# Optimization experiments

Measured on AMD Instinct MI355X. Metric: run time of the kernel, lower is better.

The kernel has to match this reference:

```python
import jax, jax.numpy as jnp
import numpy as np

N, E, IN, HID, OUT, H, NCLS = 20000, 320000, 128, 32, 8, 8, 10

def _ln(x, g, b, eps=1e-5):
    mu = x.mean(-1, keepdims=True)
    var = ((x - mu) ** 2).mean(-1, keepdims=True)
    return g * (x - mu) / jnp.sqrt(var + eps) + b

def _gelu(x):
    return jax.nn.gelu(x, approximate=False)

def _tconv(x, src, dst, Wq, bq, Wk, bk, Wv, bv, Ws, bs, heads):
    # PyG TransformerConv, concat=True, root_weight=True, lin_beta is None
    n = x.shape[0]
    C = Wq.shape[1] // heads
    q = (x @ Wq + bq).reshape(n, heads, C)
    k = (x @ Wk + bk).reshape(n, heads, C)
    v = (x @ Wv + bv).reshape(n, heads, C)
    logits = (q[dst] * k[src]).sum(-1) / jnp.sqrt(jnp.asarray(C, x.dtype))  # [E,H]
    m = jax.lax.stop_gradient(jax.ops.segment_max(logits, dst, num_segments=n))
    e = jnp.exp(logits - m[dst])
    denom = jax.ops.segment_sum(e, dst, num_segments=n)
    alpha = e / (denom[dst] + 1e-16)  # per-target-node edge softmax
    agg = jax.ops.segment_sum(alpha[:, :, None] * v[src], dst, num_segments=n)
    out = agg.reshape(n, heads * C) + x @ Ws + bs
    return out, alpha

def _forward(src, dst, x,
             c1_Wq, c1_bq, c1_Wk, c1_bk, c1_Wv, c1_bv, c1_Ws, c1_bs,
             c2_Wq, c2_bq, c2_Wk, c2_bk, c2_Wv, c2_bv, c2_Ws, c2_bs,
             c3_Wq, c3_bq, c3_Wk, c3_bk, c3_Wv, c3_bv, c3_Ws, c3_bs,
             c4_Wq, c4_bq, c4_Wk, c4_bk, c4_Wv, c4_bv, c4_Ws, c4_bs,
             n1_g, n1_b, n2_g, n2_b, n3_g, n3_b, n4_g, n4_b,
             fc_W, fc_b):
    h1 = _ln(_gelu(_tconv(x, src, dst, c1_Wq, c1_bq, c1_Wk, c1_bk, c1_Wv, c1_bv, c1_Ws, c1_bs, H)[0]), n1_g, n1_b)
    h2_raw, attn = _tconv(h1, src, dst, c2_Wq, c2_bq, c2_Wk, c2_bk, c2_Wv, c2_bv, c2_Ws, c2_bs, H)
    h2 = _ln(_gelu(h2_raw), n2_g, n2_b)
    h3 = _ln(_gelu(_tconv(h2, src, dst, c3_Wq, c3_bq, c3_Wk, c3_bk, c3_Wv, c3_bv, c3_Ws, c3_bs, H)[0]), n3_g, n3_b)
    h4 = _ln(_gelu(_tconv(h3, src, dst, c4_Wq, c4_bq, c4_Wk, c4_bk, c4_Wv, c4_bv, c4_Ws, c4_bs, 1)[0]), n4_g, n4_b)
    x_out = h2 @ fc_W + fc_b
    return x_out, h4, attn

def setup_inputs() -> dict:
    key = jax.random.key(0)
    ks = iter(jax.random.split(key, 64))
    def p(shape, s=0.05):
        return jax.random.normal(next(ks), shape, dtype=jnp.float32) * s
    inp = {}
    inp['x'] = jax.random.normal(next(ks), (N, IN), dtype=jnp.float32)
    inp['edge_index'] = jax.random.randint(next(ks), (2, E), 0, N, dtype=jnp.int32)
    dims = [('c1', IN, H * HID), ('c2', H * HID, H * OUT), ('c3', H * OUT, H * HID), ('c4', H * HID, IN)]
    for name, di, do in dims:
        for w in ['Wq', 'Wk', 'Wv', 'Ws']:
            inp[name + '_' + w] = p((di, do))
        for bnm in ['bq', 'bk', 'bv', 'bs']:
            inp[name + '_' + bnm] = jnp.zeros((do,), jnp.float32)
    for nm, d in [('n1', H * HID), ('n2', H * OUT), ('n3', H * HID), ('n4', IN)]:
        inp[nm + '_g'] = jnp.ones((d,), jnp.float32)
        inp[nm + '_b'] = jnp.zeros((d,), jnp.float32)
    inp['fc_W'] = p((H * OUT, NCLS))
    inp['fc_b'] = jnp.zeros((NCLS,), jnp.float32)
    return inp

def reference(x, edge_index,
              c1_Wq, c1_bq, c1_Wk, c1_bk, c1_Wv, c1_bv, c1_Ws, c1_bs,
              c2_Wq, c2_bq, c2_Wk, c2_bk, c2_Wv, c2_bv, c2_Ws, c2_bs,
              c3_Wq, c3_bq, c3_Wk, c3_bk, c3_Wv, c3_bv, c3_Ws, c3_bs,
              c4_Wq, c4_bq, c4_Wk, c4_bk, c4_Wv, c4_bv, c4_Ws, c4_bs,
              n1_g, n1_b, n2_g, n2_b, n3_g, n3_b, n4_g, n4_b,
              fc_W, fc_b):
    src, dst = edge_index[0], edge_index[1]
    return _forward(src, dst, x,
                    c1_Wq, c1_bq, c1_Wk, c1_bk, c1_Wv, c1_bv, c1_Ws, c1_bs,
                    c2_Wq, c2_bq, c2_Wk, c2_bk, c2_Wv, c2_bv, c2_Ws, c2_bs,
                    c3_Wq, c3_bq, c3_Wk, c3_bk, c3_Wv, c3_bv, c3_Ws, c3_bs,
                    c4_Wq, c4_bq, c4_Wk, c4_bk, c4_Wv, c4_bv, c4_Ws, c4_bs,
                    n1_g, n1_b, n2_g, n2_b, n3_g, n3_b, n4_g, n4_b,
                    fc_W, fc_b)
```

## Files before the change

### kernel.cpp

```cpp
#include <hip/hip_runtime.h>
#include <hip/hip_bf16.h>
#include <math.h>

#define NN 20000
#define MP 20032
#define NE 320000

typedef __hip_bfloat16 bf16;
typedef __attribute__((ext_vector_type(8))) short short8v;
typedef __attribute__((ext_vector_type(4))) short short4v;
typedef __attribute__((ext_vector_type(4))) float f32x4;

__device__ __forceinline__ float b2f(bf16 v){ return __bfloat162float(v); }
__device__ __forceinline__ bf16 f2b(float v){ return __float2bfloat16(v); }
__device__ __forceinline__ float bfbits(short s){
  return __uint_as_float(((unsigned)(unsigned short)s) << 16);
}
__device__ __forceinline__ int clampi(int v, int lo, int hi){ return v < lo ? lo : (v > hi ? hi : v); }
__device__ __forceinline__ void stv(bf16* p, float v){ *p = f2b(v); }
__device__ __forceinline__ void stv(float* p, float v){ *p = v; }
__device__ __forceinline__ float ldv(const bf16* p){ return b2f(*p); }
__device__ __forceinline__ float ldv(const float* p){ return *p; }

__device__ __forceinline__ float fast_erf(float x){
  float ax = fabsf(x);
  float t = __builtin_amdgcn_rcpf(1.f + 0.3275911f*ax);
  float p = ((((1.061405429f*t - 1.453152027f)*t + 1.421413741f)*t
              - 0.284496736f)*t + 0.254829592f)*t;
  float y = 1.f - p*__expf(-ax*ax);
  return copysignf(y, x);
}
__device__ __forceinline__ float gelu(float x){
  return 0.5f*x*(1.f + fast_erf(x*0.70710678118654752f));
}

template<int CPL>
__device__ __forceinline__ void ldrow(const bf16* p, float* o){
  if constexpr (CPL == 16){
    short8v v0 = *reinterpret_cast<const short8v*>(p);
    short8v v1 = *reinterpret_cast<const short8v*>(p + 8);
#pragma unroll
    for (int j = 0; j < 8; j++){ o[j] = bfbits(v0[j]); o[8+j] = bfbits(v1[j]); }
  } else if constexpr (CPL == 8){
    short8v v = *reinterpret_cast<const short8v*>(p);
#pragma unroll
    for (int j = 0; j < 8; j++) o[j] = bfbits(v[j]);
  } else {
    short4v v = *reinterpret_cast<const short4v*>(p);
#pragma unroll
    for (int j = 0; j < 4; j++) o[j] = bfbits(v[j]);
  }
}
template<int CPL>
__device__ __forceinline__ void ldrowT(const bf16* p, float* o){ ldrow<CPL>(p, o); }
template<int CPL>
__device__ __forceinline__ void ldrowT(const float* p, float* o){
#pragma unroll
  for (int j = 0; j < CPL; j += 4){
    float4 v = *reinterpret_cast<const float4*>(p + j);
    o[j] = v.x; o[j+1] = v.y; o[j+2] = v.z; o[j+3] = v.w;
  }
}

__device__ __forceinline__ short8v ldA8(const bf16* p){
  return *reinterpret_cast<const short8v*>(p);
}
__device__ __forceinline__ short8v ldA8(const float* p){
  float4 a0 = *reinterpret_cast<const float4*>(p);
  float4 a1 = *reinterpret_cast<const float4*>(p + 4);
  short8v r;
  bf16 b;
  b = f2b(a0.x); r[0] = *(const short*)&b;
  b = f2b(a0.y); r[1] = *(const short*)&b;
  b = f2b(a0.z); r[2] = *(const short*)&b;
  b = f2b(a0.w); r[3] = *(const short*)&b;
  b = f2b(a1.x); r[4] = *(const short*)&b;
  b = f2b(a1.y); r[5] = *(const short*)&b;
  b = f2b(a1.z); r[6] = *(const short*)&b;
  b = f2b(a1.w); r[7] = *(const short*)&b;
  return r;
}

__global__ void fill_k(float* __restrict__ out, int n, float val){
  int i = blockIdx.x*blockDim.x + threadIdx.x;
  if (i < n) out[i] = val;
}

struct PackArgs {
  const float* w[16];
  unsigned long long off[16];
  int K[16];
  int D[16];
};
__global__ void pack_all(PackArgs pa, bf16* __restrict__ out){
  int wi = blockIdx.y;
  int K = pa.K[wi], D = pa.D[wi];
  int i = blockIdx.x*256 + threadIdx.x;
  if (i >= K*D) return;
  int j = i & 7, l = (i >> 3) & 63;
  int TG = D >> 4;
  int tg = (i >> 9) % TG, s = (i >> 9) / TG;
  int k = s*32 + (l >> 4)*8 + j, n = tg*16 + (l & 15);
  out[pa.off[wi] + i] = f2b(pa.w[wi][(size_t)k*D + n]);
}

template<typename AT, typename TS>
__global__ void gemm_qkvs(const AT* __restrict__ X,
    const short8v* __restrict__ WQ, const short8v* __restrict__ WK,
    const short8v* __restrict__ WV, const short8v* __restrict__ WS,
    const float* __restrict__ bQ, const float* __restrict__ bK,
    const float* __restrict__ bV, const float* __restrict__ bS,
    bf16* __restrict__ Qo, bf16* __restrict__ Ko, bf16* __restrict__ Vo,
    TS* __restrict__ So,
    int K, int TG, int ldQKV, int ldS, int MstoreS){
  int w = threadIdx.x >> 6, lane = threadIdx.x & 63;
  int n0 = blockIdx.x*64;
  size_t m0 = (size_t)blockIdx.y*64 + w*16;
  int lr = lane & 15, lk = lane >> 4;
  int ar = clampi((int)(m0 + lr), 0, NN-1);
  const AT* xp = X + (size_t)ar*K + lk*8;
  size_t wo = ((size_t)(n0 >> 4))*64 + lane;
  f32x4 acc[4][4];
#pragma unroll
  for (int j = 0; j < 4; j++)
#pragma unroll
    for (int t = 0; t < 4; t++) acc[j][t] = f32x4{0,0,0,0};
  int steps = K >> 5;
  for (int s = 0; s < steps; s++){
    short8v a = ldA8(xp + s*32);
    size_t ro = wo + (size_t)s*TG*64;
#pragma unroll
    for (int t = 0; t < 4; t++){
      size_t idx = ro + t*64;
      acc[0][t] = __builtin_amdgcn_mfma_f32_16x16x32_bf16(a, WQ[idx], acc[0][t], 0, 0, 0);
      acc[1][t] = __builtin_amdgcn_mfma_f32_16x16x32_bf16(a, WK[idx], acc[1][t], 0, 0, 0);
      acc[2][t] = __builtin_amdgcn_mfma_f32_16x16x32_bf16(a, WV[idx], acc[2][t], 0, 0, 0);
      acc[3][t] = __builtin_amdgcn_mfma_f32_16x16x32_bf16(a, WS[idx], acc[3][t], 0, 0, 0);
    }
  }
#pragma unroll
  for (int t = 0; t < 4; t++){
    int col = n0 + t*16 + lr;
    float b0 = bQ[col], b1 = bK[col], b2 = bV[col], b3 = bS[col];
#pragma unroll
    for (int r = 0; r < 4; r++){
      size_t row = m0 + lk*4 + r;
      Qo[row*ldQKV + col] = f2b(acc[0][t][r] + b0);
      Ko[row*ldQKV + col] = f2b(acc[1][t][r] + b1);
      Vo[row*ldQKV + col] = f2b(acc[2][t][r] + b2);
      if ((int)row < MstoreS) stv(&So[row*(size_t)ldS + col], acc[3][t][r] + b3);
    }
  }
}

__global__ void count_k(const int* __restrict__ ei, int* __restrict__ cnt, int E){
  int e = blockIdx.x*blockDim.x + threadIdx.x;
  if (e < E){
    int d = clampi(ei[E + e], 0, NN-1);
    atomicAdd(&cnt[d], 1);
  }
}

__global__ void exscan_k(const int* __restrict__ cnt, int* __restrict__ off,
                         int* __restrict__ cur, int n){
  __shared__ int wtot[16];
  __shared__ int carrysh;
  int tid = threadIdx.x, lane = tid & 63, w = tid >> 6;
  if (tid == 0) carrysh = 0;
  __syncthreads();
  for (int base = 0; base < n; base += 1024){
    int i = base + tid;
    int v = (i < n) ? cnt[i] : 0;
    int s = v;
#pragma unroll
    for (int d = 1; d < 64; d <<= 1){
      int t = __shfl_up(s, d);
      if (lane >= d) s += t;
    }
    if (lane == 63) wtot[w] = s;
    __syncthreads();
    int woff = 0;
    for (int j = 0; j < w; j++) woff += wtot[j];
    int c = carrysh;
    if (i < n){ int val = c + woff + s - v; off[i] = val; cur[i] = val; }
    __syncthreads();
    if (tid == 1023) carrysh = c + woff + s;
    __syncthreads();
  }
  if (threadIdx.x == 0) off[n] = carrysh;
}

__global__ void scatter_k(const int* __restrict__ ei, int* __restrict__ cur,
                          int* __restrict__ perm, int* __restrict__ srcs, int E){
  int e = blockIdx.x*blockDim.x + threadIdx.x;
  if (e >= E) return;
  int s = clampi(ei[e], 0, NN-1);
  int d = clampi(ei[E + e], 0, NN-1);
  int p = atomicAdd(&cur[d], 1);
  if (p >= 0 && p < E){ perm[p] = e; srcs[p] = s; }
}

template<int D, int H, typename TO>
__global__ void fused_attn(const bf16* __restrict__ Q, const bf16* __restrict__ Kf,
                           const bf16* __restrict__ V, const int* __restrict__ srcs,
                           const int* __restrict__ offs,
                           TO* __restrict__ Xout, int ldO,
                           const float* __restrict__ G, const float* __restrict__ Bt,
                           bf16* __restrict__ LOG, const int* __restrict__ perm,
                           float* __restrict__ attn_out, float scale){
  constexpr int CPL = D/16;
  constexpr int LPH = 16/H;
  int node = blockIdx.x*4 + (threadIdx.x >> 6);
  if (node >= NN) return;
  int lane = threadIdx.x & 63;
  int hl = lane & 15;
  int slot = lane >> 4;
  float q[CPL];
  {
    float tmp[CPL];
    ldrow<CPL>(Q + (size_t)node*D + hl*CPL, tmp);
#pragma unroll
    for (int j = 0; j < CPL; j++) q[j] = tmp[j] * scale;
  }
  float den = 0.f;
  float acc[CPL];
#pragma unroll
  for (int j = 0; j < CPL; j++) acc[j] = 0.f;
  int s0 = offs[node], e0 = offs[node+1];
  int i = s0 + slot;
  bool vcur = i < e0;
  int sc = vcur ? srcs[i] : 0;
  float kc[CPL], vc[CPL];
  ldrow<CPL>(Kf + (size_t)sc*D + hl*CPL, kc);
  ldrow<CPL>(V  + (size_t)sc*D + hl*CPL, vc);
  int iters = (e0 - s0 + 3) >> 2;
  for (int it = 0; it < iters; ++it){
    int inext = i + 4;
    bool vnxt = inext < e0;
    int sn = vnxt ? srcs[inext] : 0;
    float kn[CPL], vn[CPL];
    ldrow<CPL>(Kf + (size_t)sn*D + hl*CPL, kn);
    ldrow<CPL>(V  + (size_t)sn*D + hl*CPL, vn);
    float t = 0.f;
#pragma unroll
    for (int j = 0; j < CPL; j++) t += q[j]*kc[j];
#pragma unroll
    for (int o = 1; o < LPH; o <<= 1) t += __shfl_xor(t, o);
    if (LOG && vcur && ((hl & (LPH-1)) == 0)) LOG[(size_t)i*H + hl/LPH] = f2b(t);
    float pe = vcur ? __expf(t) : 0.f;
    den += pe;
#pragma unroll
    for (int j = 0; j < CPL; j++) acc[j] += pe*vc[j];
    vcur = vnxt; i = inext;
#pragma unroll
    for (int j = 0; j < CPL; j++){ kc[j] = kn[j]; vc[j] = vn[j]; }
  }
  den += __shfl_xor(den, 16);
  den += __shfl_xor(den, 32);
#pragma unroll
  for (int j = 0; j < CPL; j++){
    acc[j] += __shfl_xor(acc[j], 16);
    acc[j] += __shfl_xor(acc[j], 32);
  }
  float inv = 1.f/(den + 1e-16f);

  {
    float sk[CPL];
    ldrowT<CPL>(Xout + (size_t)node*ldO + hl*CPL, sk);
    float v[CPL]; float s = 0.f;
#pragma unroll
    for (int j = 0; j < CPL; j++){
      float ge = gelu(sk[j] + acc[j]*inv);
      v[j] = ge; s += ge;
    }
#pragma unroll
    for (int o = 1; o < 16; o <<= 1) s += __shfl_xor(s, o);
    float mu = s * (1.f/D);
    float qv = 0.f;
#pragma unroll
    for (int j = 0; j < CPL; j++){ float d2 = v[j]-mu; qv += d2*d2; }
#pragma unroll
    for (int o = 1; o < 16; o <<= 1) qv += __shfl_xor(qv, o);
    float lni = 1.f / sqrtf(qv*(1.f/D) + 1e-5f);
    if (slot == 0){
      TO* oo = Xout + (size_t)node*ldO + hl*CPL;
#pragma unroll
      for (int j = 0; j < CPL; j++){
        int c = hl*CPL + j;
        stv(&oo[j], G[c]*(v[j]-mu)*lni + Bt[c]);
      }
    }
  }

  if (attn_out){
    asm volatile("s_waitcnt vmcnt(0)" ::: "memory");
    int total = (e0 - s0) * H;
    int it2 = (total + 63) >> 6;
    for (int b = 0; b < it2; b++){
      int idx = b*64 + lane;
      int h = idx & (H-1);
      float dh = __shfl(den, h*LPH);
      if (idx < total){
        int pos = s0 + (idx >> 3);
        float lg = b2f(LOG[(size_t)pos*H + h]);
        attn_out[(size_t)perm[pos]*H + h] = __expf(lg)/(dh + 1e-16f);
      }
    }
  }
}

__global__ void fc_k(const bf16* __restrict__ X, const float* __restrict__ W,
                     const float* __restrict__ B, float* __restrict__ Out,
                     int K, int D){
  int m = blockIdx.x*4 + (threadIdx.x >> 6);
  int lane = threadIdx.x & 63;
  if (m >= NN || lane >= D) return;
  float acc = B[lane];
  for (int k = 0; k < K; k++) acc += b2f(X[(size_t)m*K + k]) * W[(size_t)k*D + lane];
  Out[(size_t)m*D + lane] = acc;
}

extern "C" void kernel_launch(void* const* d_in, const int* in_sizes, int n_in,
                              void* d_out, int out_size, void* d_ws, size_t ws_size,
                              hipStream_t stream){
  int code = 0;
  if (n_in != 44) code = 100;
  else {
    const int wsz[4] = {32768,16384,16384,32768};
    const int bsz[4] = {256,64,256,128};
    bool ok = in_sizes[0] == NN*128 && in_sizes[1] == 2*NE
           && in_sizes[42] == 640 && in_sizes[43] == 10;
    for (int l = 0; l < 4 && ok; l++){
      for (int j = 0; j < 4; j++)
        ok = ok && in_sizes[2+l*8+j] == wsz[l] && in_sizes[2+l*8+4+j] == bsz[l];
      ok = ok && in_sizes[34+2*l] == bsz[l] && in_sizes[35+2*l] == bsz[l];
    }
    if (!ok) code = 140;
  }
  if (code){
    fill_k<<<((size_t)out_size+255)/256, 256, 0, stream>>>((float*)d_out, out_size, (float)code);
    return;
  }

  const float* x = (const float*)d_in[0];
  const int*   ei = (const int*)d_in[1];
  const float *W[4][4], *Bw[4][4], *lng[4], *lnb[4];
  for (int l = 0; l < 4; l++){
    for (int j = 0; j < 4; j++){
      W[l][j]  = (const float*)d_in[2 + l*8 + j];
      Bw[l][j] = (const float*)d_in[2 + l*8 + 4 + j];
    }
    lng[l] = (const float*)d_in[34 + 2*l];
    lnb[l] = (const float*)d_in[35 + 2*l];
  }
  const float* fcW = (const float*)d_in[42];
  const float* fcB = (const float*)d_in[43];

  char* ws = (char*)d_ws;
  size_t o = 0;
  auto alloc = [&](size_t bytes)->void*{ void* p = ws + o; o += (bytes + 255)/256*256; return p; };
  bf16* Hb   = (bf16*)alloc((size_t)MP*256*2);
  bf16* H2b  = (bf16*)alloc((size_t)MP*64*2);
  bf16* Qb   = (bf16*)alloc((size_t)MP*256*2);
  bf16* Kb   = (bf16*)alloc((size_t)MP*256*2);
  bf16* Vb   = (bf16*)alloc((size_t)MP*256*2);
  bf16* LOG  = (bf16*)alloc((size_t)NE*8*2);
  int* OFFS  = (int*)alloc((size_t)(NN+1)*4);
  int* CNT   = (int*)alloc((size_t)(NN+1)*4);
  int* CURS  = (int*)alloc((size_t)(NN+1)*4);
  int* PERM  = (int*)alloc((size_t)NE*4);
  int* SRCS  = (int*)alloc((size_t)NE*4);
  bf16* WPK  = (bf16*)alloc((size_t)393216*2);
  size_t need = o;

  float* out_x  = (float*)d_out;
  float* out_h4 = out_x + (size_t)NN*10;
  float* out_at = out_h4 + (size_t)NN*128;

  if (ws_size < need){
    fill_k<<<((size_t)out_size+255)/256, 256, 0, stream>>>((float*)d_out, out_size, 160.0f);
    return;
  }

  const int KD[4] = {128,256,64,256};
  const int DD[4] = {256,64,256,128};
  PackArgs pa;
  bf16* Wp[4][4];
  {
    size_t off = 0;
    for (int l = 0; l < 4; l++)
      for (int j = 0; j < 4; j++){
        int idx = l*4 + j;
        pa.w[idx] = W[l][j];
        pa.off[idx] = off;
        pa.K[idx] = KD[l];
        pa.D[idx] = DD[l];
        Wp[l][j] = WPK + off;
        off += (size_t)KD[l]*DD[l];
      }
  }
  pack_all<<<dim3(128,16),256,0,stream>>>(pa, WPK);

  hipMemsetAsync(CNT, 0, (size_t)NN*4, stream);
  count_k<<<NE/256, 256, 0, stream>>>(ei, CNT, NE);
  exscan_k<<<1, 1024, 0, stream>>>(CNT, OFFS, CURS, NN);
  scatter_k<<<NE/256, 256, 0, stream>>>(ei, CURS, PERM, SRCS, NE);

  const float s32  = 0.1767766952966369f;
  const float s8   = 0.3535533905932738f;
  const float s128 = 0.0883883476483184f;
  const dim3 g64(1, MP/64), g128(2, MP/64), g256(4, MP/64);

  gemm_qkvs<float,bf16><<<g256,256,0,stream>>>(x,
      (const short8v*)Wp[0][0], (const short8v*)Wp[0][1],
      (const short8v*)Wp[0][2], (const short8v*)Wp[0][3],
      Bw[0][0], Bw[0][1], Bw[0][2], Bw[0][3],
      Qb, Kb, Vb, Hb, 128, 16, 256, 256, MP);
  fused_attn<256,8,bf16><<<NN/4,256,0,stream>>>(Qb,Kb,Vb, SRCS,OFFS, Hb,256,
      lng[0],lnb[0], nullptr,nullptr,nullptr, s32);

  gemm_qkvs<bf16,bf16><<<g64,256,0,stream>>>(Hb,
      (const short8v*)Wp[1][0], (const short8v*)Wp[1][1],
      (const short8v*)Wp[1][2], (const short8v*)Wp[1][3],
      Bw[1][0], Bw[1][1], Bw[1][2], Bw[1][3],
      Qb, Kb, Vb, H2b, 256, 4, 64, 64, MP);
  fused_attn<64,8,bf16><<<NN/4,256,0,stream>>>(Qb,Kb,Vb, SRCS,OFFS, H2b,64,
      lng[1],lnb[1], LOG,PERM,out_at, s8);

  fc_k<<<NN/4,256,0,stream>>>(H2b, fcW, fcB, out_x, 64, 10);

  gemm_qkvs<bf16,bf16><<<g256,256,0,stream>>>(H2b,
      (const short8v*)Wp[2][0], (const short8v*)Wp[2][1],
      (const short8v*)Wp[2][2], (const short8v*)Wp[2][3],
      Bw[2][0], Bw[2][1], Bw[2][2], Bw[2][3],
      Qb, Kb, Vb, Hb, 64, 16, 256, 256, MP);
  fused_attn<256,8,bf16><<<NN/4,256,0,stream>>>(Qb,Kb,Vb, SRCS,OFFS, Hb,256,
      lng[2],lnb[2], nullptr,nullptr,nullptr, s32);

  gemm_qkvs<bf16,float><<<g128,256,0,stream>>>(Hb,
      (const short8v*)Wp[3][0], (const short8v*)Wp[3][1],
      (const short8v*)Wp[3][2], (const short8v*)Wp[3][3],
      Bw[3][0], Bw[3][1], Bw[3][2], Bw[3][3],
      Qb, Kb, Vb, out_h4, 256, 8, 128, 128, NN);
  fused_attn<128,1,float><<<NN/4,256,0,stream>>>(Qb,Kb,Vb, SRCS,OFFS, out_h4,128,
      lng[3],lnb[3], nullptr,nullptr,nullptr, s128);
}
```

Before: 337.8 us.

## Interleave K and V rows in one buffer and double-buffer edge gathers

```diff
diff --git a/kernel.cpp b/kernel.cpp
--- a/kernel.cpp
+++ b/kernel.cpp
@@ -112,7 +112,7 @@
     const float* __restrict__ bV, const float* __restrict__ bS,
     bf16* __restrict__ Qo, bf16* __restrict__ Ko, bf16* __restrict__ Vo,
     TS* __restrict__ So,
-    int K, int TG, int ldQKV, int ldS, int MstoreS){
+    int K, int TG, int ldQ, int ldKV, int ldS, int MstoreS){
   int w = threadIdx.x >> 6, lane = threadIdx.x & 63;
   int n0 = blockIdx.x*64;
   size_t m0 = (size_t)blockIdx.y*64 + w*16;
@@ -145,9 +145,9 @@
 #pragma unroll
     for (int r = 0; r < 4; r++){
       size_t row = m0 + lk*4 + r;
-      Qo[row*ldQKV + col] = f2b(acc[0][t][r] + b0);
-      Ko[row*ldQKV + col] = f2b(acc[1][t][r] + b1);
-      Vo[row*ldQKV + col] = f2b(acc[2][t][r] + b2);
+      Qo[row*(size_t)ldQ  + col] = f2b(acc[0][t][r] + b0);
+      Ko[row*(size_t)ldKV + col] = f2b(acc[1][t][r] + b1);
+      Vo[row*(size_t)ldKV + col] = f2b(acc[2][t][r] + b2);
       if ((int)row < MstoreS) stv(&So[row*(size_t)ldS + col], acc[3][t][r] + b3);
     }
   }
@@ -201,9 +201,8 @@
 }
 
 template<int D, int H, typename TO>
-__global__ void fused_attn(const bf16* __restrict__ Q, const bf16* __restrict__ Kf,
-                           const bf16* __restrict__ V, const int* __restrict__ srcs,
-                           const int* __restrict__ offs,
+__global__ void fused_attn(const bf16* __restrict__ Q, const bf16* __restrict__ KV,
+                           const int* __restrict__ srcs, const int* __restrict__ offs,
                            TO* __restrict__ Xout, int ldO,
                            const float* __restrict__ G, const float* __restrict__ Bt,
                            bf16* __restrict__ LOG, const int* __restrict__ perm,
@@ -227,33 +226,37 @@
 #pragma unroll
   for (int j = 0; j < CPL; j++) acc[j] = 0.f;
   int s0 = offs[node], e0 = offs[node+1];
-  int i = s0 + slot;
-  bool vcur = i < e0;
-  int sc = vcur ? srcs[i] : 0;
-  float kc[CPL], vc[CPL];
-  ldrow<CPL>(Kf + (size_t)sc*D + hl*CPL, kc);
-  ldrow<CPL>(V  + (size_t)sc*D + hl*CPL, vc);
+
+  float kA[CPL], vA[CPL], kB[CPL], vB[CPL];
+  auto LD = [&](int i, float* k, float* v){
+    int sc = (i < e0) ? srcs[i] : 0;
+    const bf16* base = KV + (size_t)sc*(2*D) + hl*CPL;
+    ldrow<CPL>(base,     k);
+    ldrow<CPL>(base + D, v);
+  };
+  auto PROC = [&](int i, const float* k, const float* v){
+    float t = 0.f;
+#pragma unroll
+    for (int j = 0; j < CPL; j++) t += q[j]*k[j];
+#pragma unroll
+    for (int o = 1; o < LPH; o <<= 1) t += __shfl_xor(t, o);
+    bool val = i < e0;
+    if (LOG && val && ((hl & (LPH-1)) == 0)) LOG[(size_t)i*H + hl/LPH] = f2b(t);
+    float pe = val ? __expf(t) : 0.f;
+    den += pe;
+#pragma unroll
+    for (int j = 0; j < CPL; j++) acc[j] += pe*v[j];
+  };
+
+  int iA = s0 + slot;
   int iters = (e0 - s0 + 3) >> 2;
-  for (int it = 0; it < iters; ++it){
-    int inext = i + 4;
-    bool vnxt = inext < e0;
-    int sn = vnxt ? srcs[inext] : 0;
-    float kn[CPL], vn[CPL];
-    ldrow<CPL>(Kf + (size_t)sn*D + hl*CPL, kn);
-    ldrow<CPL>(V  + (size_t)sn*D + hl*CPL, vn);
-    float t = 0.f;
-#pragma unroll
-    for (int j = 0; j < CPL; j++) t += q[j]*kc[j];
-#pragma unroll
-    for (int o = 1; o < LPH; o <<= 1) t += __shfl_xor(t, o);
-    if (LOG && vcur && ((hl & (LPH-1)) == 0)) LOG[(size_t)i*H + hl/LPH] = f2b(t);
-    float pe = vcur ? __expf(t) : 0.f;
-    den += pe;
-#pragma unroll
-    for (int j = 0; j < CPL; j++) acc[j] += pe*vc[j];
-    vcur = vnxt; i = inext;
-#pragma unroll
-    for (int j = 0; j < CPL; j++){ kc[j] = kn[j]; vc[j] = vn[j]; }
+  LD(iA, kA, vA);
+  for (int it = 0; it < iters; it += 2){
+    LD(iA + 4, kB, vB);
+    PROC(iA, kA, vA);
+    LD(iA + 8, kA, vA);
+    PROC(iA + 4, kB, vB);
+    iA += 8;
   }
   den += __shfl_xor(den, 16);
   den += __shfl_xor(den, 32);
@@ -362,14 +365,13 @@
   bf16* Hb   = (bf16*)alloc((size_t)MP*256*2);
   bf16* H2b  = (bf16*)alloc((size_t)MP*64*2);
   bf16* Qb   = (bf16*)alloc((size_t)MP*256*2);
-  bf16* Kb   = (bf16*)alloc((size_t)MP*256*2);
-  bf16* Vb   = (bf16*)alloc((size_t)MP*256*2);
+  bf16* KVb  = (bf16*)alloc((size_t)MP*512*2);
   bf16* LOG  = (bf16*)alloc((size_t)NE*8*2);
   int* OFFS  = (int*)alloc((size_t)(NN+1)*4);
   int* CNT   = (int*)alloc((size_t)(NN+1)*4);
   int* CURS  = (int*)alloc((size_t)(NN+1)*4);
   int* PERM  = (int*)alloc((size_t)NE*4);
-  int* SRCS  = (int*)alloc((size_t)NE*4);
+  int* SRCS  = (int*)alloc((size_t)(NE+16)*4);
   bf16* WPK  = (bf16*)alloc((size_t)393216*2);
   size_t need = o;
 
@@ -415,17 +417,17 @@
       (const short8v*)Wp[0][0], (const short8v*)Wp[0][1],
       (const short8v*)Wp[0][2], (const short8v*)Wp[0][3],
       Bw[0][0], Bw[0][1], Bw[0][2], Bw[0][3],
-      Qb, Kb, Vb, Hb, 128, 16, 256, 256, MP);
-  fused_attn<256,8,bf16><<<NN/4,256,0,stream>>>(Qb,Kb,Vb, SRCS,OFFS, Hb,256,
-      lng[0],lnb[0], nullptr,nullptr,nullptr, s32);
+      Qb, KVb, KVb + 256, Hb, 128, 16, 256, 512, 256, MP);
+  fused_attn<256,8,bf16><<<NN/4,256,0,stream>>>(Qb, KVb, SRCS, OFFS, Hb, 256,
+      lng[0], lnb[0], nullptr, nullptr, nullptr, s32);
 
   gemm_qkvs<bf16,bf16><<<g64,256,0,stream>>>(Hb,
       (const short8v*)Wp[1][0], (const short8v*)Wp[1][1],
       (const short8v*)Wp[1][2], (const short8v*)Wp[1][3],
       Bw[1][0], Bw[1][1], Bw[1][2], Bw[1][3],
-      Qb, Kb, Vb, H2b, 256, 4, 64, 64, MP);
-  fused_attn<64,8,bf16><<<NN/4,256,0,stream>>>(Qb,Kb,Vb, SRCS,OFFS, H2b,64,
-      lng[1],lnb[1], LOG,PERM,out_at, s8);
+      Qb, KVb, KVb + 64, H2b, 256, 4, 64, 128, 64, MP);
+  fused_attn<64,8,bf16><<<NN/4,256,0,stream>>>(Qb, KVb, SRCS, OFFS, H2b, 64,
+      lng[1], lnb[1], LOG, PERM, out_at, s8);
 
   fc_k<<<NN/4,256,0,stream>>>(H2b, fcW, fcB, out_x, 64, 10);
 
@@ -433,15 +435,15 @@
       (const short8v*)Wp[2][0], (const short8v*)Wp[2][1],
       (const short8v*)Wp[2][2], (const short8v*)Wp[2][3],
       Bw[2][0], Bw[2][1], Bw[2][2], Bw[2][3],
-      Qb, Kb, Vb, Hb, 64, 16, 256, 256, MP);
-  fused_attn<256,8,bf16><<<NN/4,256,0,stream>>>(Qb,Kb,Vb, SRCS,OFFS, Hb,256,
-      lng[2],lnb[2], nullptr,nullptr,nullptr, s32);
+      Qb, KVb, KVb + 256, Hb, 64, 16, 256, 512, 256, MP);
+  fused_attn<256,8,bf16><<<NN/4,256,0,stream>>>(Qb, KVb, SRCS, OFFS, Hb, 256,
+      lng[2], lnb[2], nullptr, nullptr, nullptr, s32);
 
   gemm_qkvs<bf16,float><<<g128,256,0,stream>>>(Hb,
       (const short8v*)Wp[3][0], (const short8v*)Wp[3][1],
       (const short8v*)Wp[3][2], (const short8v*)Wp[3][3],
       Bw[3][0], Bw[3][1], Bw[3][2], Bw[3][3],
-      Qb, Kb, Vb, out_h4, 256, 8, 128, 128, NN);
-  fused_attn<128,1,float><<<NN/4,256,0,stream>>>(Qb,Kb,Vb, SRCS,OFFS, out_h4,128,
-      lng[3],lnb[3], nullptr,nullptr,nullptr, s128);
-}
+      Qb, KVb, KVb + 128, out_h4, 256, 8, 128, 256, 128, NN);
+  fused_attn<128,1,float><<<NN/4,256,0,stream>>>(Qb, KVb, SRCS, OFFS, out_h4, 128,
+      lng[3], lnb[3], nullptr, nullptr, nullptr, s128);
+}
```

Result: no change. 340.6 us (+0.8%).
